# Optimization experiments

Measured on AMD Instinct MI355X. Metric: run time of the kernel, lower is better.

## Reference

```python
import jax, jax.numpy as jnp
import numpy as np

N, D, S, P = 768, 64, 32, 4
RBF_START, RBF_END = 0.0, 12.0
ENERGY_SCALE = 1.0


def setup_inputs() -> dict:
    key = jax.random.key(0)
    k = jax.random.split(key, 4)
    hid = jax.random.normal(k[0], (N, D), jnp.float32)
    # coords spread out so pairwise distances span the RBF range [0, 12]
    coords = jax.random.normal(k[1], (P, N, 3), jnp.float32) * 4.0
    W_rbf = jax.random.normal(k[2], (D, D, S), jnp.float32) / D
    b_rbf = jax.random.normal(k[3], (S,), jnp.float32) * 0.01
    weight = jnp.ones((1,), jnp.float32)
    bias = jnp.zeros((1,), jnp.float32)
    return {"hid": hid, "coords": coords, "W_rbf": W_rbf, "b_rbf": b_rbf,
            "weight": weight, "bias": bias}


def reference(hid, coords, W_rbf, b_rbf, weight, bias):
    # --- interaction matrix: einsum('xi,yj->xyij') + Linear(D*D -> S), fused ---
    # identical math to reshape(N,N,D*D) @ W.reshape(D*D,S) + b
    inter = jnp.einsum('xi,yj,ijs->xys', hid, hid, W_rbf) + b_rbf  # [N,N,S]

    # --- cdist_diff: pairwise euclidean distances per pose ---
    diff = coords[:, :, None, :] - coords[:, None, :, :]           # [P,N,N,3]
    dists = jnp.sqrt(jnp.sum(diff * diff, axis=-1) + 1e-12)        # [P,N,N]

    # --- rbf_encode: gaussian basis over [RBF_START, RBF_END] with S steps ---
    mu = jnp.linspace(RBF_START, RBF_END, S, dtype=jnp.float32)    # [S]
    sigma = (RBF_END - RBF_START) / S
    rbfs = jnp.exp(-((dists[..., None] - mu) ** 2) / (2.0 * sigma * sigma))  # [P,N,N,S]

    # --- masked interaction energy (exclude self-pairs) ---
    inv_ident = (~jnp.eye(N, dtype=bool))[None, :, :, None]        # [1,N,N,1]
    interact = inter[None] * rbfs * ENERGY_SCALE
    interact = jnp.where(inv_ident, interact, 0.0)
    U = interact.mean(axis=(-3, -2, -1)) * weight[0] + bias[0]     # [P]
    return U
```

## Files before the change

### kernel.cpp

```cpp
#include <hip/hip_runtime.h>
#include <hip/hip_bf16.h>
#include <math.h>

#define NN 768
#define DD 64
#define SS 32
#define PP 4

#define MU_STEP   (12.0f / 31.0f)
#define INV2SIG2  3.55555555555f

__global__ __launch_bounds__(256) void k1_T(const float* __restrict__ hid,
                                            const float* __restrict__ W,
                                            float* __restrict__ T) {
    const int b   = blockIdx.x;
    const int cb  = b & 3;
    const int xb  = b >> 2;
    const int c0  = cb * 512;
    const int x0  = xb * 16;
    const int tid = threadIdx.x;
    const int ct  = tid & 63;
    const int xt  = tid >> 6;

    __shared__ float hs[16 * 64];
    {
        const float4 v = *reinterpret_cast<const float4*>(&hid[(size_t)x0 * 64 + tid * 4]);
        float4* dst = reinterpret_cast<float4*>(&hs[tid * 4]);
        *dst = v;
    }
    __syncthreads();

    float acc[4][8];
#pragma unroll
    for (int m = 0; m < 4; ++m)
#pragma unroll
        for (int u = 0; u < 8; ++u) acc[m][u] = 0.0f;

    const int cbase = c0 + ct * 8;
#pragma unroll 4
    for (int i = 0; i < 64; ++i) {
        const float4 w0 = *reinterpret_cast<const float4*>(&W[(size_t)i * 2048 + cbase]);
        const float4 w1 = *reinterpret_cast<const float4*>(&W[(size_t)i * 2048 + cbase + 4]);
#pragma unroll
        for (int m = 0; m < 4; ++m) {
            const float hm = hs[(xt * 4 + m) * 64 + i];
            acc[m][0] += hm * w0.x;
            acc[m][1] += hm * w0.y;
            acc[m][2] += hm * w0.z;
            acc[m][3] += hm * w0.w;
            acc[m][4] += hm * w1.x;
            acc[m][5] += hm * w1.y;
            acc[m][6] += hm * w1.z;
            acc[m][7] += hm * w1.w;
        }
    }

#pragma unroll
    for (int m = 0; m < 4; ++m) {
        const int x = x0 + xt * 4 + m;
        float4 o0, o1;
        o0.x = acc[m][0]; o0.y = acc[m][1]; o0.z = acc[m][2]; o0.w = acc[m][3];
        o1.x = acc[m][4]; o1.y = acc[m][5]; o1.z = acc[m][6]; o1.w = acc[m][7];
        *reinterpret_cast<float4*>(&T[(size_t)x * 2048 + cbase])     = o0;
        *reinterpret_cast<float4*>(&T[(size_t)x * 2048 + cbase + 4]) = o1;
    }
}

template <bool USE_WS_T>
__global__ __launch_bounds__(256) void k2_main(const float* __restrict__ hid,
                                               const float* __restrict__ coords,
                                               const float* __restrict__ W,
                                               const float* __restrict__ b_rbf,
                                               const float* __restrict__ Tg,
                                               float* __restrict__ partials) {
    const int x   = blockIdx.x;
    const int tid = threadIdx.x;
    const int ty  = tid & 63;
    const int ts  = tid >> 6;

    __shared__ float T_l[2048];
    __shared__ float h_t[64 * 192];
    __shared__ float4 red[256];
    __shared__ float hx[64];

    if (USE_WS_T) {
        const float4 a = *reinterpret_cast<const float4*>(&Tg[(size_t)x * 2048 + tid * 8]);
        const float4 b = *reinterpret_cast<const float4*>(&Tg[(size_t)x * 2048 + tid * 8 + 4]);
        *reinterpret_cast<float4*>(&T_l[tid * 8])     = a;
        *reinterpret_cast<float4*>(&T_l[tid * 8 + 4]) = b;
    } else {
        if (tid < 64) hx[tid] = hid[(size_t)x * 64 + tid];
        __syncthreads();
        float a0[4] = {0, 0, 0, 0}, a1[4] = {0, 0, 0, 0};
        for (int i = 0; i < 64; ++i) {
            const float hv = hx[i];
            const float4 w0 = *reinterpret_cast<const float4*>(&W[(size_t)i * 2048 + tid * 4]);
            const float4 w1 = *reinterpret_cast<const float4*>(&W[(size_t)i * 2048 + 1024 + tid * 4]);
            a0[0] += hv * w0.x; a0[1] += hv * w0.y; a0[2] += hv * w0.z; a0[3] += hv * w0.w;
            a1[0] += hv * w1.x; a1[1] += hv * w1.y; a1[2] += hv * w1.z; a1[3] += hv * w1.w;
        }
        T_l[tid * 4 + 0] = a0[0]; T_l[tid * 4 + 1] = a0[1];
        T_l[tid * 4 + 2] = a0[2]; T_l[tid * 4 + 3] = a0[3];
        T_l[1024 + tid * 4 + 0] = a1[0]; T_l[1024 + tid * 4 + 1] = a1[1];
        T_l[1024 + tid * 4 + 2] = a1[2]; T_l[1024 + tid * 4 + 3] = a1[3];
    }

    float mu_reg[8], b_reg[8];
#pragma unroll
    for (int u = 0; u < 8; ++u) {
        const int s = ts * 8 + u;
        mu_reg[u] = (float)s * MU_STEP;
        b_reg[u]  = b_rbf[s];
    }
    float cx[PP][3];
#pragma unroll
    for (int p = 0; p < PP; ++p)
#pragma unroll
        for (int c = 0; c < 3; ++c)
            cx[p][c] = coords[(size_t)p * NN * 3 + (size_t)x * 3 + c];

    float e[PP] = {0.0f, 0.0f, 0.0f, 0.0f};

    for (int ch = 0; ch < 4; ++ch) {
        const int yc = ch * 192;
        __syncthreads();
        if (tid < 192) {
            const int y = yc + tid;
#pragma unroll
            for (int r = 0; r < 16; ++r) {
                const float4 v = *reinterpret_cast<const float4*>(&hid[(size_t)y * 64 + r * 4]);
                h_t[(r * 4 + 0) * 192 + tid] = v.x;
                h_t[(r * 4 + 1) * 192 + tid] = v.y;
                h_t[(r * 4 + 2) * 192 + tid] = v.z;
                h_t[(r * 4 + 3) * 192 + tid] = v.w;
            }
        }
        __syncthreads();

        float acc[3][8];
#pragma unroll
        for (int i = 0; i < 3; ++i)
#pragma unroll
            for (int u = 0; u < 8; ++u) acc[i][u] = 0.0f;

#pragma unroll 4
        for (int j = 0; j < 64; ++j) {
            const float h0 = h_t[j * 192 + ty * 3 + 0];
            const float h1 = h_t[j * 192 + ty * 3 + 1];
            const float h2 = h_t[j * 192 + ty * 3 + 2];
            const float4 t0 = *reinterpret_cast<const float4*>(&T_l[j * 32 + ts * 8]);
            const float4 t1 = *reinterpret_cast<const float4*>(&T_l[j * 32 + ts * 8 + 4]);
            acc[0][0] += h0 * t0.x; acc[0][1] += h0 * t0.y; acc[0][2] += h0 * t0.z; acc[0][3] += h0 * t0.w;
            acc[0][4] += h0 * t1.x; acc[0][5] += h0 * t1.y; acc[0][6] += h0 * t1.z; acc[0][7] += h0 * t1.w;
            acc[1][0] += h1 * t0.x; acc[1][1] += h1 * t0.y; acc[1][2] += h1 * t0.z; acc[1][3] += h1 * t0.w;
            acc[1][4] += h1 * t1.x; acc[1][5] += h1 * t1.y; acc[1][6] += h1 * t1.z; acc[1][7] += h1 * t1.w;
            acc[2][0] += h2 * t0.x; acc[2][1] += h2 * t0.y; acc[2][2] += h2 * t0.z; acc[2][3] += h2 * t0.w;
            acc[2][4] += h2 * t1.x; acc[2][5] += h2 * t1.y; acc[2][6] += h2 * t1.z; acc[2][7] += h2 * t1.w;
        }

#pragma unroll
        for (int i = 0; i < 3; ++i) {
            const int y = yc + ty * 3 + i;
            if (y == x) continue;
#pragma unroll
            for (int p = 0; p < PP; ++p) {
                const float dx = cx[p][0] - coords[(size_t)p * NN * 3 + (size_t)y * 3 + 0];
                const float dy = cx[p][1] - coords[(size_t)p * NN * 3 + (size_t)y * 3 + 1];
                const float dz = cx[p][2] - coords[(size_t)p * NN * 3 + (size_t)y * 3 + 2];
                const float d  = sqrtf(dx * dx + dy * dy + dz * dz + 1e-12f);
                float ep = 0.0f;
#pragma unroll
                for (int u = 0; u < 8; ++u) {
                    const float t = d - mu_reg[u];
                    const float w = __expf(-(t * t) * INV2SIG2);
                    ep += (acc[i][u] + b_reg[u]) * w;
                }
                e[p] += ep;
            }
        }
    }

    __syncthreads();
    float4 ev; ev.x = e[0]; ev.y = e[1]; ev.z = e[2]; ev.w = e[3];
    red[tid] = ev;
    __syncthreads();
#pragma unroll
    for (int st = 128; st >= 1; st >>= 1) {
        if (tid < st) {
            float4 a = red[tid], b = red[tid + st];
            a.x += b.x; a.y += b.y; a.z += b.z; a.w += b.w;
            red[tid] = a;
        }
        __syncthreads();
    }
    if (tid == 0) *reinterpret_cast<float4*>(&partials[(size_t)x * 4]) = red[0];
}

__global__ __launch_bounds__(256) void k3_final(const float* __restrict__ partials,
                                                const float* __restrict__ weight,
                                                const float* __restrict__ bias_,
                                                float* __restrict__ out) {
    const int p    = threadIdx.x >> 6;
    const int lane = threadIdx.x & 63;
    float s = 0.0f;
#pragma unroll
    for (int k = 0; k < 12; ++k) s += partials[(size_t)(lane * 12 + k) * 4 + p];
#pragma unroll
    for (int off = 1; off < 64; off <<= 1) s += __shfl_xor(s, off, 64);
    if (lane == 0)
        out[p] = s * (1.0f / 18874368.0f) * weight[0] + bias_[0];
}

extern "C" void kernel_launch(void* const* d_in, const int* in_sizes, int n_in,
                              void* d_out, int out_size, void* d_ws, size_t ws_size,
                              hipStream_t stream) {
    const float* hid    = (const float*)d_in[0];
    const float* coords = (const float*)d_in[1];
    const float* W      = (const float*)d_in[2];
    const float* b_rbf  = (const float*)d_in[3];
    const float* weight = (const float*)d_in[4];
    const float* bias_  = (const float*)d_in[5];
    float* out = (float*)d_out;

    const size_t T_BYTES    = (size_t)NN * 2048 * sizeof(float);
    const size_t PART_BYTES = (size_t)NN * 4 * sizeof(float);
    const bool use_ws = ws_size >= T_BYTES + PART_BYTES;

    float* Tg       = (float*)d_ws;
    float* partials = use_ws ? (float*)((char*)d_ws + T_BYTES) : (float*)d_ws;

    if (use_ws) {
        k1_T<<<192, 256, 0, stream>>>(hid, W, Tg);
        k2_main<true><<<NN, 256, 0, stream>>>(hid, coords, W, b_rbf, Tg, partials);
    } else {
        k2_main<false><<<NN, 256, 0, stream>>>(hid, coords, W, b_rbf, nullptr, partials);
    }
    k3_final<<<1, 256, 0, stream>>>(partials, weight, bias_, out);
}
```

Before: 82.11 us.

## Fuse final reduction into main kernel and shrink y-chunk tiling

The final reduction is folded into the main kernel through an atomic ticket counter: the last block to finish sums all partials, so the separate finalize launch is gone. The block reduction now uses wavefront shuffles instead of a shared-memory tree, and the exponential becomes exp2 with a folded constant and fma. The y tile shrinks from 192 to 128 rows with 2 rows per thread, which lowers LDS use and registers so 4 blocks can fit per CU. The risks are the extra atomic and fences, and fewer FMAs per thread per chunk.

Measured after the change: 121.0 us. 47.4% more time.

```diff
diff --git a/kernel.cpp b/kernel.cpp
--- a/kernel.cpp
+++ b/kernel.cpp
@@ -9,10 +9,14 @@
 
 #define MU_STEP   (12.0f / 31.0f)
 #define INV2SIG2  3.55555555555f
+#define NEG2C     (-INV2SIG2 * 1.4426950408889634f)
 
 __global__ __launch_bounds__(256) void k1_T(const float* __restrict__ hid,
                                             const float* __restrict__ W,
-                                            float* __restrict__ T) {
+                                            float* __restrict__ T,
+                                            unsigned* __restrict__ ctr) {
+    if (blockIdx.x == 0 && threadIdx.x == 0) *ctr = 0u;
+
     const int b   = blockIdx.x;
     const int cb  = b & 3;
     const int xb  = b >> 2;
@@ -25,8 +29,7 @@
     __shared__ float hs[16 * 64];
     {
         const float4 v = *reinterpret_cast<const float4*>(&hid[(size_t)x0 * 64 + tid * 4]);
-        float4* dst = reinterpret_cast<float4*>(&hs[tid * 4]);
-        *dst = v;
+        *reinterpret_cast<float4*>(&hs[tid * 4]) = v;
     }
     __syncthreads();
 
@@ -44,14 +47,10 @@
 #pragma unroll
         for (int m = 0; m < 4; ++m) {
             const float hm = hs[(xt * 4 + m) * 64 + i];
-            acc[m][0] += hm * w0.x;
-            acc[m][1] += hm * w0.y;
-            acc[m][2] += hm * w0.z;
-            acc[m][3] += hm * w0.w;
-            acc[m][4] += hm * w1.x;
-            acc[m][5] += hm * w1.y;
-            acc[m][6] += hm * w1.z;
-            acc[m][7] += hm * w1.w;
+            acc[m][0] += hm * w0.x; acc[m][1] += hm * w0.y;
+            acc[m][2] += hm * w0.z; acc[m][3] += hm * w0.w;
+            acc[m][4] += hm * w1.x; acc[m][5] += hm * w1.y;
+            acc[m][6] += hm * w1.z; acc[m][7] += hm * w1.w;
         }
     }
 
@@ -67,21 +66,24 @@
 }
 
 template <bool USE_WS_T>
-__global__ __launch_bounds__(256) void k2_main(const float* __restrict__ hid,
-                                               const float* __restrict__ coords,
-                                               const float* __restrict__ W,
-                                               const float* __restrict__ b_rbf,
-                                               const float* __restrict__ Tg,
-                                               float* __restrict__ partials) {
+__global__ __launch_bounds__(256, 4) void k2_main(const float* __restrict__ hid,
+                                                  const float* __restrict__ coords,
+                                                  const float* __restrict__ W,
+                                                  const float* __restrict__ b_rbf,
+                                                  const float* __restrict__ Tg,
+                                                  float* __restrict__ partials,
+                                                  unsigned* __restrict__ ctr,
+                                                  const float* __restrict__ weight,
+                                                  const float* __restrict__ bias_,
+                                                  float* __restrict__ out) {
     const int x   = blockIdx.x;
     const int tid = threadIdx.x;
     const int ty  = tid & 63;
     const int ts  = tid >> 6;
 
-    __shared__ float T_l[2048];
-    __shared__ float h_t[64 * 192];
-    __shared__ float4 red[256];
-    __shared__ float hx[64];
+    __shared__ float pool[2048 + 64 * 128];
+    float* T_l = pool;
+    float* h_t = pool + 2048;
 
     if (USE_WS_T) {
         const float4 a = *reinterpret_cast<const float4*>(&Tg[(size_t)x * 2048 + tid * 8]);
@@ -89,11 +91,9 @@
         *reinterpret_cast<float4*>(&T_l[tid * 8])     = a;
         *reinterpret_cast<float4*>(&T_l[tid * 8 + 4]) = b;
     } else {
-        if (tid < 64) hx[tid] = hid[(size_t)x * 64 + tid];
-        __syncthreads();
         float a0[4] = {0, 0, 0, 0}, a1[4] = {0, 0, 0, 0};
         for (int i = 0; i < 64; ++i) {
-            const float hv = hx[i];
+            const float hv = hid[(size_t)x * 64 + i];
             const float4 w0 = *reinterpret_cast<const float4*>(&W[(size_t)i * 2048 + tid * 4]);
             const float4 w1 = *reinterpret_cast<const float4*>(&W[(size_t)i * 2048 + 1024 + tid * 4]);
             a0[0] += hv * w0.x; a0[1] += hv * w0.y; a0[2] += hv * w0.z; a0[3] += hv * w0.w;
@@ -121,46 +121,56 @@
 
     float e[PP] = {0.0f, 0.0f, 0.0f, 0.0f};
 
-    for (int ch = 0; ch < 4; ++ch) {
-        const int yc = ch * 192;
-        __syncthreads();
-        if (tid < 192) {
-            const int y = yc + tid;
-#pragma unroll
-            for (int r = 0; r < 16; ++r) {
-                const float4 v = *reinterpret_cast<const float4*>(&hid[(size_t)y * 64 + r * 4]);
-                h_t[(r * 4 + 0) * 192 + tid] = v.x;
-                h_t[(r * 4 + 1) * 192 + tid] = v.y;
-                h_t[(r * 4 + 2) * 192 + tid] = v.z;
-                h_t[(r * 4 + 3) * 192 + tid] = v.w;
+    const int srow = tid >> 1;
+    const int r0   = (tid & 1) * 8;
+    const int hoff = ty * 2;
+    const int toff = ts * 8;
+
+    for (int ch = 0; ch < 6; ++ch) {
+        const int y0 = ch * 128;
+        __syncthreads();
+        {
+            const int y = y0 + srow;
+#pragma unroll
+            for (int r = 0; r < 8; ++r) {
+                const float4 v = *reinterpret_cast<const float4*>(
+                    &hid[(size_t)y * 64 + (r0 + r) * 4]);
+                const int j = (r0 + r) * 4;
+                h_t[(j + 0) * 128 + srow] = v.x;
+                h_t[(j + 1) * 128 + srow] = v.y;
+                h_t[(j + 2) * 128 + srow] = v.z;
+                h_t[(j + 3) * 128 + srow] = v.w;
             }
         }
         __syncthreads();
 
-        float acc[3][8];
-#pragma unroll
-        for (int i = 0; i < 3; ++i)
+        float acc[2][8];
+#pragma unroll
+        for (int i = 0; i < 2; ++i)
 #pragma unroll
             for (int u = 0; u < 8; ++u) acc[i][u] = 0.0f;
 
 #pragma unroll 4
         for (int j = 0; j < 64; ++j) {
-            const float h0 = h_t[j * 192 + ty * 3 + 0];
-            const float h1 = h_t[j * 192 + ty * 3 + 1];
-            const float h2 = h_t[j * 192 + ty * 3 + 2];
-            const float4 t0 = *reinterpret_cast<const float4*>(&T_l[j * 32 + ts * 8]);
-            const float4 t1 = *reinterpret_cast<const float4*>(&T_l[j * 32 + ts * 8 + 4]);
+            const float h0 = h_t[j * 128 + hoff];
+            const float h1 = h_t[j * 128 + hoff + 1];
+            const float4 t0 = *reinterpret_cast<const float4*>(&T_l[j * 32 + toff]);
+            const float4 t1 = *reinterpret_cast<const float4*>(&T_l[j * 32 + toff + 4]);
             acc[0][0] += h0 * t0.x; acc[0][1] += h0 * t0.y; acc[0][2] += h0 * t0.z; acc[0][3] += h0 * t0.w;
             acc[0][4] += h0 * t1.x; acc[0][5] += h0 * t1.y; acc[0][6] += h0 * t1.z; acc[0][7] += h0 * t1.w;
             acc[1][0] += h1 * t0.x; acc[1][1] += h1 * t0.y; acc[1][2] += h1 * t0.z; acc[1][3] += h1 * t0.w;
             acc[1][4] += h1 * t1.x; acc[1][5] += h1 * t1.y; acc[1][6] += h1 * t1.z; acc[1][7] += h1 * t1.w;
-            acc[2][0] += h2 * t0.x; acc[2][1] += h2 * t0.y; acc[2][2] += h2 * t0.z; acc[2][3] += h2 * t0.w;
-            acc[2][4] += h2 * t1.x; acc[2][5] += h2 * t1.y; acc[2][6] += h2 * t1.z; acc[2][7] += h2 * t1.w;
-        }
-
-#pragma unroll
-        for (int i = 0; i < 3; ++i) {
-            const int y = yc + ty * 3 + i;
+        }
+
+        float ab[2][8];
+#pragma unroll
+        for (int i = 0; i < 2; ++i)
+#pragma unroll
+            for (int u = 0; u < 8; ++u) ab[i][u] = acc[i][u] + b_reg[u];
+
+#pragma unroll
+        for (int i = 0; i < 2; ++i) {
+            const int y = y0 + hoff + i;
             if (y == x) continue;
 #pragma unroll
             for (int p = 0; p < PP; ++p) {
@@ -172,28 +182,54 @@
 #pragma unroll
                 for (int u = 0; u < 8; ++u) {
                     const float t = d - mu_reg[u];
-                    const float w = __expf(-(t * t) * INV2SIG2);
-                    ep += (acc[i][u] + b_reg[u]) * w;
+                    const float w = __builtin_exp2f(t * t * NEG2C);
+                    ep = fmaf(ab[i][u], w, ep);
                 }
                 e[p] += ep;
             }
         }
     }
 
+#pragma unroll
+    for (int off = 1; off < 64; off <<= 1)
+#pragma unroll
+        for (int p = 0; p < PP; ++p) e[p] += __shfl_xor(e[p], off, 64);
+
     __syncthreads();
-    float4 ev; ev.x = e[0]; ev.y = e[1]; ev.z = e[2]; ev.w = e[3];
-    red[tid] = ev;
+    if (ty == 0) {
+#pragma unroll
+        for (int p = 0; p < PP; ++p) pool[ts * 4 + p] = e[p];
+    }
     __syncthreads();
-#pragma unroll
-    for (int st = 128; st >= 1; st >>= 1) {
-        if (tid < st) {
-            float4 a = red[tid], b = red[tid + st];
-            a.x += b.x; a.y += b.y; a.z += b.z; a.w += b.w;
-            red[tid] = a;
-        }
-        __syncthreads();
-    }
-    if (tid == 0) *reinterpret_cast<float4*>(&partials[(size_t)x * 4]) = red[0];
+    if (tid < 4) {
+        const float s = pool[0 * 4 + tid] + pool[1 * 4 + tid] +
+                        pool[2 * 4 + tid] + pool[3 * 4 + tid];
+        partials[(size_t)x * 4 + tid] = s;
+    }
+
+    if (USE_WS_T) {
+        __threadfence();
+        __syncthreads();
+        unsigned* flag = reinterpret_cast<unsigned*>(&pool[16]);
+        if (tid == 0) {
+            const unsigned old = atomicAdd(ctr, 1u);
+            *flag = (old == NN - 1) ? 1u : 0u;
+        }
+        __syncthreads();
+        if (*flag) {
+            __threadfence();
+            const int p    = tid >> 6;
+            const int lane = tid & 63;
+            float s = 0.0f;
+#pragma unroll
+            for (int k = 0; k < 12; ++k)
+                s += partials[(size_t)(lane * 12 + k) * 4 + p];
+#pragma unroll
+            for (int off = 1; off < 64; off <<= 1) s += __shfl_xor(s, off, 64);
+            if (lane == 0)
+                out[p] = s * (1.0f / 18874368.0f) * weight[0] + bias_[0];
+        }
+    }
 }
 
 __global__ __launch_bounds__(256) void k3_final(const float* __restrict__ partials,
@@ -224,16 +260,19 @@
 
     const size_t T_BYTES    = (size_t)NN * 2048 * sizeof(float);
     const size_t PART_BYTES = (size_t)NN * 4 * sizeof(float);
-    const bool use_ws = ws_size >= T_BYTES + PART_BYTES;
-
-    float* Tg       = (float*)d_ws;
-    float* partials = use_ws ? (float*)((char*)d_ws + T_BYTES) : (float*)d_ws;
+    const bool use_ws = ws_size >= T_BYTES + PART_BYTES + 64;
+
+    float*    Tg       = (float*)d_ws;
+    float*    partials = use_ws ? (float*)((char*)d_ws + T_BYTES) : (float*)d_ws;
+    unsigned* ctr      = (unsigned*)((char*)d_ws + T_BYTES + PART_BYTES);
 
     if (use_ws) {
-        k1_T<<<192, 256, 0, stream>>>(hid, W, Tg);
-        k2_main<true><<<NN, 256, 0, stream>>>(hid, coords, W, b_rbf, Tg, partials);
+        k1_T<<<192, 256, 0, stream>>>(hid, W, Tg, ctr);
+        k2_main<true><<<NN, 256, 0, stream>>>(hid, coords, W, b_rbf, Tg, partials,
+                                              ctr, weight, bias_, out);
     } else {
-        k2_main<false><<<NN, 256, 0, stream>>>(hid, coords, W, b_rbf, nullptr, partials);
-    }
-    k3_final<<<1, 256, 0, stream>>>(partials, weight, bias_, out);
-}
+        k2_main<false><<<NN, 256, 0, stream>>>(hid, coords, W, b_rbf, nullptr, partials,
+                                               nullptr, weight, bias_, out);
+        k3_final<<<1, 256, 0, stream>>>(partials, weight, bias_, out);
+    }
+}
```
